# Optimization experiments

Measured on AMD Instinct MI355X. Metric: run time of the kernel, lower is better.

## Reference

```python
import jax, jax.numpy as jnp
import numpy as np
import math

HIDDEN = 1024
HEADS = 16
HEAD_DIM = HIDDEN // HEADS
B, S = 2, 2048


def setup_inputs() -> dict:
    key = jax.random.key(0)
    ks = jax.random.split(key, 10)
    std = 1.0 / math.sqrt(HIDDEN)
    mk = lambda k: (jax.random.normal(k, (HIDDEN, HIDDEN), jnp.float32) * std)
    return {
        "hidden_states": jax.random.normal(ks[0], (B, S, HIDDEN), jnp.float32),
        "attention_mask": jnp.zeros((B, 1, 1, S), jnp.float32),
        "wq": mk(ks[1]), "bq": jnp.zeros((HIDDEN,), jnp.float32),
        "wk": mk(ks[2]), "bk": jnp.zeros((HIDDEN,), jnp.float32),
        "wv": mk(ks[3]), "bv": jnp.zeros((HIDDEN,), jnp.float32),
        "wo": mk(ks[4]), "bo": jnp.zeros((HIDDEN,), jnp.float32),
    }


def reference(hidden_states, attention_mask, wq, bq, wk, bk, wv, bv, wo, bo):
    b, s, _ = hidden_states.shape
    scale = math.sqrt(HEAD_DIM)
    # projections (torch Linear: x @ W.T + b); weights stored as [out, in]
    q = hidden_states @ wq.T + bq
    k = hidden_states @ wk.T + bk
    v = hidden_states @ wv.T + bv
    # [B, H, S, D]
    q = q.reshape(b, s, HEADS, HEAD_DIM).transpose(0, 2, 1, 3)
    k = k.reshape(b, s, HEADS, HEAD_DIM).transpose(0, 2, 1, 3)
    v = v.reshape(b, s, HEADS, HEAD_DIM).transpose(0, 2, 1, 3)
    scores = jnp.einsum("bhqd,bhkd->bhqk", q, k) / scale
    scores = scores + attention_mask  # broadcast [B,1,1,S]
    weights = jax.nn.softmax(scores, axis=-1)  # dropout = identity (eval)
    out = jnp.einsum("bhqk,bhkd->bhqd", weights, v)
    out = out.transpose(0, 2, 1, 3).reshape(b, s, HIDDEN)
    out = out @ wo.T + bo
    return out
```

## Files before the change

kernel.cpp:

```cpp
#include <hip/hip_runtime.h>
#include <hip/hip_bf16.h>

typedef __bf16 bf16_t;
typedef __bf16 bf16x8 __attribute__((ext_vector_type(8)));
typedef _Float16 f16x4 __attribute__((ext_vector_type(4)));
typedef _Float16 f16x8 __attribute__((ext_vector_type(8)));
typedef float f32x4 __attribute__((ext_vector_type(4)));

#define SEQ    2048
#define NH     16
#define HD     64
#define HIDDEN 1024
#define LOG2E  1.44269504f
#define CSTR   41

__device__ __forceinline__ bf16_t to_bf16(float f) { return (bf16_t)f; }

__device__ __forceinline__ void async16(const void* g, void* l) {
    __builtin_amdgcn_global_load_lds((const __attribute__((address_space(1))) void*)g,
                                     (__attribute__((address_space(3))) void*)l, 16, 0, 0);
}

__global__ __launch_bounds__(256) void cvt_kernel(
    const float* __restrict__ s0, bf16_t* __restrict__ d0, int c0,
    const float* __restrict__ s1, bf16_t* __restrict__ d1, int c1,
    const float* __restrict__ s2, bf16_t* __restrict__ d2, int c2,
    const float* __restrict__ s3, bf16_t* __restrict__ d3, int c3,
    const float* __restrict__ s4, bf16_t* __restrict__ d4, int c4)
{
    int blk = blockIdx.x;
    const float* s; bf16_t* d;
    if (blk < c0)              { s = s0; d = d0; }
    else if ((blk -= c0) < c1) { s = s1; d = d1; }
    else if ((blk -= c1) < c2) { s = s2; d = d2; }
    else if ((blk -= c2) < c3) { s = s3; d = d3; }
    else                       { blk -= c3; s = s4; d = d4; }
    const size_t base = (size_t)blk * 2048 + threadIdx.x * 8;
    const float4 a = *(const float4*)&s[base];
    const float4 b = *(const float4*)&s[base + 4];
    bf16x8 o;
    o[0] = (bf16_t)a.x; o[1] = (bf16_t)a.y; o[2] = (bf16_t)a.z; o[3] = (bf16_t)a.w;
    o[4] = (bf16_t)b.x; o[5] = (bf16_t)b.y; o[6] = (bf16_t)b.z; o[7] = (bf16_t)b.w;
    *(bf16x8*)&d[base] = o;
}

__global__ __launch_bounds__(256, 3) void qkv_kernel(
    const bf16_t* __restrict__ X,
    const bf16_t* __restrict__ wq, const bf16_t* __restrict__ wk, const bf16_t* __restrict__ wv,
    const float* __restrict__ bq, const float* __restrict__ bk, const float* __restrict__ bv,
    bf16_t* __restrict__ qws, bf16_t* __restrict__ kws, _Float16* __restrict__ vws)
{
    __shared__ __align__(16) bf16_t Sh[16384];
    const int z = blockIdx.z;
    const bf16_t* Wsel = (z == 0) ? wq : (z == 1) ? wk : wv;
    const float*  bsel = (z == 0) ? bq : (z == 1) ? bk : bv;
    const int m0 = blockIdx.y * 128, n0 = blockIdx.x * 128;

    const int t = threadIdx.x, lane = t & 63, w = t >> 6;
    const int w0 = w & 1, w1 = w >> 1, l15 = lane & 15, q4 = lane >> 4;

    f32x4 acc[4][4];
#pragma unroll
    for (int i = 0; i < 4; i++)
#pragma unroll
        for (int j = 0; j < 4; j++) acc[i][j] = f32x4{0.f, 0.f, 0.f, 0.f};

    auto stage = [&](int kt, int buf) {
#pragma unroll
        for (int j = 0; j < 2; j++) {
            const int s = j * 256 + t;
            const int row = s >> 2, c = (s & 3) ^ (row & 3);
            const int lb = buf * 8192 + (j * 256 + w * 64) * 8;
            async16(&X[(size_t)(m0 + row) * HIDDEN + kt + c * 8], &Sh[lb]);
            async16(&Wsel[(size_t)(n0 + row) * HIDDEN + kt + c * 8], &Sh[lb + 4096]);
        }
    };
    stage(0, 0);

    for (int it = 0; it < 32; it++) {
        const int cur = it & 1;
        __syncthreads();
        if (it < 31) stage((it + 1) * 32, cur ^ 1);
        const bf16_t* As = &Sh[cur * 8192];
        const bf16_t* Bs = &Sh[cur * 8192 + 4096];
        bf16x8 af[4];
#pragma unroll
        for (int ti = 0; ti < 4; ti++) {
            const int ra = w0 * 64 + ti * 16 + l15;
            af[ti] = *(const bf16x8*)&As[ra * 32 + (q4 ^ (ra & 3)) * 8];
        }
#pragma unroll
        for (int tj = 0; tj < 4; tj++) {
            const int rb = w1 * 64 + tj * 16 + l15;
            const bf16x8 bfr = *(const bf16x8*)&Bs[rb * 32 + (q4 ^ (rb & 3)) * 8];
#pragma unroll
            for (int ti = 0; ti < 4; ti++)
                acc[ti][tj] = __builtin_amdgcn_mfma_f32_16x16x32_bf16(af[ti], bfr, acc[ti][tj], 0, 0, 0);
        }
    }
    __syncthreads();

    if (z < 2) {
#pragma unroll
        for (int tj = 0; tj < 4; tj++) {
            const int n = w1 * 64 + tj * 16 + l15;
            const float bb = bsel[n0 + n];
            const int ch = (n >> 3), sub = n & 7;
#pragma unroll
            for (int ti = 0; ti < 4; ti++)
#pragma unroll
                for (int r = 0; r < 4; r++) {
                    const int m = w0 * 64 + ti * 16 + q4 * 4 + r;
                    Sh[m * 128 + ((ch ^ (m & 15)) << 3) + sub] = to_bf16(acc[ti][tj][r] + bb);
                }
        }
        __syncthreads();
        bf16_t* dst = (z == 0) ? qws : kws;
#pragma unroll
        for (int i = 0; i < 8; i++) {
            const int g = i * 256 + t;
            const int row = g >> 4, c = g & 15;
            const bf16x8 vv = *(const bf16x8*)&Sh[row * 128 + ((c ^ (row & 15)) << 3)];
            *(bf16x8*)&dst[(size_t)(m0 + row) * HIDDEN + n0 + c * 8] = vv;
        }
    } else {
        _Float16* Vt = (_Float16*)Sh;
#pragma unroll
        for (int tj = 0; tj < 4; tj++) {
            const int n = w1 * 64 + tj * 16 + l15;
            const float bb = bsel[n0 + n];
#pragma unroll
            for (int ti = 0; ti < 4; ti++) {
                const int mb = w0 * 64 + ti * 16 + q4 * 4;
                f16x4 v;
#pragma unroll
                for (int r = 0; r < 4; r++) v[r] = (_Float16)(acc[ti][tj][r] + bb);
                *(f16x4*)&Vt[n * 128 + (((mb >> 3) ^ (n & 15)) << 3) + (mb & 7)] = v;
            }
        }
        __syncthreads();
        const int b = m0 >> 11, sbase = m0 & (SEQ - 1);
#pragma unroll
        for (int i = 0; i < 8; i++) {
            const int g = i * 256 + t;
            const int row = g >> 4, c = g & 15;
            const f16x8 vv = *(const f16x8*)&Vt[row * 128 + ((c ^ (row & 15)) << 3)];
            const int d = (n0 + row) & 63, hh = (n0 + row) >> 6;
            *(f16x8*)&vws[(((size_t)b * NH + hh) * HD + d) * SEQ + sbase + c * 8] = vv;
        }
    }
}

__global__ __launch_bounds__(256, 4) void attn_kernel(
    const bf16_t* __restrict__ Qw, const bf16_t* __restrict__ Kw,
    const _Float16* __restrict__ Vtw, const float* __restrict__ Mask,
    bf16_t* __restrict__ Ow)
{
    __shared__ __align__(16) bf16_t Tiles[2][2][64 * 64];

    const int t = threadIdx.x, lane = t & 63, w = t >> 6;
    const int l15 = lane & 15, q4 = lane >> 4;
    const int wq = w & 1, kh = w >> 1;
    const int lid = blockIdx.x;
    const int c8 = lid & 7, j = lid >> 3;
    const int bh = c8 * 4 + (j >> 5);
    const int q0 = (j & 31) * 64;
    const int b = bh >> 4, h = bh & 15;

    const bf16_t* Qh = Qw + (size_t)b * SEQ * HIDDEN + h * HD;
    const bf16_t* Kh = Kw + (size_t)b * SEQ * HIDDEN + h * HD;
    const _Float16* Vh = Vtw + (size_t)bh * HD * SEQ;
    const float* Mrow = Mask + (size_t)b * SEQ;

    bf16x8 qf[2][2];
#pragma unroll
    for (int nq = 0; nq < 2; nq++)
#pragma unroll
        for (int ks = 0; ks < 2; ks++)
            qf[nq][ks] = *(const bf16x8*)&Qh[(size_t)(q0 + wq * 32 + nq * 16 + l15) * HIDDEN + ks * 32 + q4 * 8];

    f32x4 oacc[2][4];
#pragma unroll
    for (int nq = 0; nq < 2; nq++)
#pragma unroll
        for (int nb = 0; nb < 4; nb++) oacc[nq][nb] = f32x4{0.f, 0.f, 0.f, 0.f};
    float psum[2] = {0.f, 0.f};

    bf16_t* Ksh = &Tiles[kh][0][0];
    _Float16* Vsh = (_Float16*)&Tiles[kh][1][0];
    const int kbase = kh * (SEQ / 2);
    const int s0_ = wq * 64 + lane;

    for (int it = 0; it < 16; it++) {
        const int kt = kbase + it * 64;
#pragma unroll
        for (int jj = 0; jj < 4; jj++) {
            const int s = jj * 128 + s0_;
            const int row = s >> 3, c = (s & 7) ^ (row & 7);
            const int lbase = (jj * 128 + wq * 64) * 8;
            async16(&Kh[(size_t)(kt + row) * HIDDEN + c * 8], &Ksh[lbase]);
            async16(&Vh[(size_t)row * SEQ + kt + c * 8], &Vsh[lbase]);
        }
        __syncthreads();

        f32x4 sa[2][4];
#pragma unroll
        for (int nq = 0; nq < 2; nq++)
#pragma unroll
            for (int cb = 0; cb < 4; cb++) sa[nq][cb] = f32x4{0.f, 0.f, 0.f, 0.f};
#pragma unroll
        for (int cb = 0; cb < 4; cb++)
#pragma unroll
            for (int ks = 0; ks < 2; ks++) {
                const int rk = cb * 16 + l15;
                const bf16x8 kf = *(const bf16x8*)&Ksh[rk * 64 + (((ks * 4 + q4) ^ (rk & 7))) * 8];
                sa[0][cb] = __builtin_amdgcn_mfma_f32_16x16x32_bf16(kf, qf[0][ks], sa[0][cb], 0, 0, 0);
                sa[1][cb] = __builtin_amdgcn_mfma_f32_16x16x32_bf16(kf, qf[1][ks], sa[1][cb], 0, 0, 0);
            }

        f16x4 ph[2][4];
#pragma unroll
        for (int cb = 0; cb < 4; cb++) {
            float4 mv = *(const float4*)&Mrow[kt + cb * 16 + q4 * 4];
            mv.x *= LOG2E; mv.y *= LOG2E; mv.z *= LOG2E; mv.w *= LOG2E;
            const float mk[4] = {mv.x, mv.y, mv.z, mv.w};
#pragma unroll
            for (int nq = 0; nq < 2; nq++) {
#pragma unroll
                for (int r = 0; r < 4; r++) {
                    const float p = exp2f(fmaf(sa[nq][cb][r], 0.125f * LOG2E, mk[r]));
                    psum[nq] += p;
                    ph[nq][cb][r] = (_Float16)p;
                }
            }
        }

#pragma unroll
        for (int cb = 0; cb < 4; cb++) {
#pragma unroll
            for (int nb = 0; nb < 4; nb++) {
                const int rv = nb * 16 + l15;
                const int cl = (cb * 2 + (q4 >> 1)) ^ (rv & 7);
                const f16x4 vf = *(const f16x4*)&Vsh[rv * 64 + cl * 8 + (q4 & 1) * 4];
                oacc[0][nb] = __builtin_amdgcn_mfma_f32_16x16x16f16(ph[0][cb], vf, oacc[0][nb], 0, 0, 0);
                oacc[1][nb] = __builtin_amdgcn_mfma_f32_16x16x16f16(ph[1][cb], vf, oacc[1][nb], 0, 0, 0);
            }
        }
        __syncthreads();
    }

#pragma unroll
    for (int nq = 0; nq < 2; nq++) {
        psum[nq] += __shfl_xor(psum[nq], 16);
        psum[nq] += __shfl_xor(psum[nq], 32);
    }

    float* Cb = (float*)&Tiles[0][0][0];
    const int crow = (wq * 64 + lane) * CSTR;
    if (kh == 1) {
#pragma unroll
        for (int nq = 0; nq < 2; nq++) {
#pragma unroll
            for (int nb = 0; nb < 4; nb++)
                *(f32x4*)&Cb[crow + (nq * 4 + nb) * 4] = oacc[nq][nb];
            Cb[crow + 32 + nq] = psum[nq];
        }
    }
    __syncthreads();
    if (kh == 0) {
#pragma unroll
        for (int nq = 0; nq < 2; nq++) {
#pragma unroll
            for (int nb = 0; nb < 4; nb++)
                oacc[nq][nb] += *(const f32x4*)&Cb[crow + (nq * 4 + nb) * 4];
            psum[nq] += Cb[crow + 32 + nq];
        }
#pragma unroll
        for (int nq = 0; nq < 2; nq++) {
            float inv[4];
#pragma unroll
            for (int r = 0; r < 4; r++) inv[r] = 1.f / __shfl(psum[nq], q4 * 4 + r);
#pragma unroll
            for (int r = 0; r < 4; r++) {
                const int s = q0 + wq * 32 + nq * 16 + q4 * 4 + r;
#pragma unroll
                for (int nb = 0; nb < 4; nb++)
                    Ow[((size_t)b * SEQ + s) * HIDDEN + h * HD + nb * 16 + l15] =
                        to_bf16(oacc[nq][nb][r] * inv[r]);
            }
        }
    }
}

__global__ __launch_bounds__(256, 2) void oproj_kernel(
    const bf16_t* __restrict__ A, const bf16_t* __restrict__ Wo,
    const float* __restrict__ bo, float* __restrict__ Out)
{
    __shared__ __align__(16) bf16_t Sh[12288];
    const int m0 = blockIdx.y * 64, n0 = blockIdx.x * 128;
    const int t = threadIdx.x, lane = t & 63, w = t >> 6;
    const int l15 = lane & 15, q4 = lane >> 4;

    f32x4 acc[4][2];
#pragma unroll
    for (int i = 0; i < 4; i++)
#pragma unroll
        for (int j = 0; j < 2; j++) acc[i][j] = f32x4{0.f, 0.f, 0.f, 0.f};

    auto stage = [&](int kt, int buf) {
        {
            const int row = t >> 2, c = (t & 3) ^ (row & 3);
            async16(&A[(size_t)(m0 + row) * HIDDEN + kt + c * 8], &Sh[buf * 6144 + w * 64 * 8]);
        }
#pragma unroll
        for (int j = 0; j < 2; j++) {
            const int s = j * 256 + t;
            const int row = s >> 2, c = (s & 3) ^ (row & 3);
            async16(&Wo[(size_t)(n0 + row) * HIDDEN + kt + c * 8],
                    &Sh[buf * 6144 + 2048 + (j * 256 + w * 64) * 8]);
        }
    };
    stage(0, 0);

    for (int it = 0; it < 32; it++) {
        const int cur = it & 1;
        __syncthreads();
        if (it < 31) stage((it + 1) * 32, cur ^ 1);
        const bf16_t* As = &Sh[cur * 6144];
        const bf16_t* Bs = &Sh[cur * 6144 + 2048];
        bf16x8 af[4];
#pragma unroll
        for (int ti = 0; ti < 4; ti++) {
            const int ra = ti * 16 + l15;
            af[ti] = *(const bf16x8*)&As[ra * 32 + (q4 ^ (ra & 3)) * 8];
        }
#pragma unroll
        for (int tj = 0; tj < 2; tj++) {
            const int rb = w * 32 + tj * 16 + l15;
            const bf16x8 bfr = *(const bf16x8*)&Bs[rb * 32 + (q4 ^ (rb & 3)) * 8];
#pragma unroll
            for (int ti = 0; ti < 4; ti++)
                acc[ti][tj] = __builtin_amdgcn_mfma_f32_16x16x32_bf16(bfr, af[ti], acc[ti][tj], 0, 0, 0);
        }
    }

#pragma unroll
    for (int tj = 0; tj < 2; tj++) {
        const int nb4 = n0 + w * 32 + tj * 16 + q4 * 4;
        const float4 bb = *(const float4*)&bo[nb4];
#pragma unroll
        for (int ti = 0; ti < 4; ti++) {
            const int m = m0 + ti * 16 + l15;
            float4 ov;
            ov.x = acc[ti][tj][0] + bb.x;
            ov.y = acc[ti][tj][1] + bb.y;
            ov.z = acc[ti][tj][2] + bb.z;
            ov.w = acc[ti][tj][3] + bb.w;
            *(float4*)&Out[(size_t)m * HIDDEN + nb4] = ov;
        }
    }
}

extern "C" void kernel_launch(void* const* d_in, const int* in_sizes, int n_in,
                              void* d_out, int out_size, void* d_ws, size_t ws_size,
                              hipStream_t stream) {
    const float* X   = (const float*)d_in[0];
    const float* msk = (const float*)d_in[1];
    const float* wq  = (const float*)d_in[2];
    const float* bq  = (const float*)d_in[3];
    const float* wk  = (const float*)d_in[4];
    const float* bk  = (const float*)d_in[5];
    const float* wv  = (const float*)d_in[6];
    const float* bv  = (const float*)d_in[7];
    const float* wo  = (const float*)d_in[8];
    const float* bo  = (const float*)d_in[9];
    float* out = (float*)d_out;

    const size_t NELT = (size_t)2 * SEQ * HIDDEN;
    const size_t WELT = (size_t)HIDDEN * HIDDEN;
    bf16_t*    xbf = (bf16_t*)d_ws;
    bf16_t*    qws = xbf + NELT;
    bf16_t*    kws = qws + NELT;
    _Float16*  vws = (_Float16*)(kws + NELT);
    bf16_t*    aws = xbf;
    bf16_t*    wqb = (bf16_t*)d_out;
    bf16_t*    wkb = wqb + WELT;
    bf16_t*    wvb = wkb + WELT;
    bf16_t*    wob = wvb + WELT;

    cvt_kernel<<<dim3(2048 + 4 * 512), dim3(256), 0, stream>>>(
        X, xbf, 2048, wq, wqb, 512, wk, wkb, 512, wv, wvb, 512, wo, wob, 512);
    qkv_kernel<<<dim3(8, 32, 3), dim3(256), 0, stream>>>(
        xbf, wqb, wkb, wvb, bq, bk, bv, qws, kws, vws);
    attn_kernel<<<dim3(1024), dim3(256), 0, stream>>>(qws, kws, vws, msk, aws);
    oproj_kernel<<<dim3(8, 64), dim3(256), 0, stream>>>(aws, wob, bo, out);
}
```

Baseline: 208.4 us.

## Fuse fp32 weight conversion into QKV and output-projection GEMM tile loads

```diff
diff --git a/kernel.cpp b/kernel.cpp
--- a/kernel.cpp
+++ b/kernel.cpp
@@ -21,39 +21,35 @@
                                      (__attribute__((address_space(3))) void*)l, 16, 0, 0);
 }
 
+__device__ __forceinline__ bf16x8 pack_bf16(const f32x4 a, const f32x4 b) {
+    bf16x8 o;
+    o[0] = (bf16_t)a[0]; o[1] = (bf16_t)a[1]; o[2] = (bf16_t)a[2]; o[3] = (bf16_t)a[3];
+    o[4] = (bf16_t)b[0]; o[5] = (bf16_t)b[1]; o[6] = (bf16_t)b[2]; o[7] = (bf16_t)b[3];
+    return o;
+}
+
 __global__ __launch_bounds__(256) void cvt_kernel(
-    const float* __restrict__ s0, bf16_t* __restrict__ d0, int c0,
-    const float* __restrict__ s1, bf16_t* __restrict__ d1, int c1,
-    const float* __restrict__ s2, bf16_t* __restrict__ d2, int c2,
-    const float* __restrict__ s3, bf16_t* __restrict__ d3, int c3,
-    const float* __restrict__ s4, bf16_t* __restrict__ d4, int c4)
+    const float* __restrict__ s0, bf16_t* __restrict__ d0)
 {
-    int blk = blockIdx.x;
-    const float* s; bf16_t* d;
-    if (blk < c0)              { s = s0; d = d0; }
-    else if ((blk -= c0) < c1) { s = s1; d = d1; }
-    else if ((blk -= c1) < c2) { s = s2; d = d2; }
-    else if ((blk -= c2) < c3) { s = s3; d = d3; }
-    else                       { blk -= c3; s = s4; d = d4; }
-    const size_t base = (size_t)blk * 2048 + threadIdx.x * 8;
-    const float4 a = *(const float4*)&s[base];
-    const float4 b = *(const float4*)&s[base + 4];
+    const size_t base = (size_t)blockIdx.x * 2048 + threadIdx.x * 8;
+    const float4 a = *(const float4*)&s0[base];
+    const float4 b = *(const float4*)&s0[base + 4];
     bf16x8 o;
     o[0] = (bf16_t)a.x; o[1] = (bf16_t)a.y; o[2] = (bf16_t)a.z; o[3] = (bf16_t)a.w;
     o[4] = (bf16_t)b.x; o[5] = (bf16_t)b.y; o[6] = (bf16_t)b.z; o[7] = (bf16_t)b.w;
-    *(bf16x8*)&d[base] = o;
+    *(bf16x8*)&d0[base] = o;
 }
 
 __global__ __launch_bounds__(256, 3) void qkv_kernel(
     const bf16_t* __restrict__ X,
-    const bf16_t* __restrict__ wq, const bf16_t* __restrict__ wk, const bf16_t* __restrict__ wv,
+    const float* __restrict__ wq, const float* __restrict__ wk, const float* __restrict__ wv,
     const float* __restrict__ bq, const float* __restrict__ bk, const float* __restrict__ bv,
     bf16_t* __restrict__ qws, bf16_t* __restrict__ kws, _Float16* __restrict__ vws)
 {
-    __shared__ __align__(16) bf16_t Sh[16384];
+    __shared__ __align__(16) bf16_t Sh[24576];
     const int z = blockIdx.z;
-    const bf16_t* Wsel = (z == 0) ? wq : (z == 1) ? wk : wv;
-    const float*  bsel = (z == 0) ? bq : (z == 1) ? bk : bv;
+    const float* Wsel = (z == 0) ? wq : (z == 1) ? wk : wv;
+    const float* bsel = (z == 0) ? bq : (z == 1) ? bk : bv;
     const int m0 = blockIdx.y * 128, n0 = blockIdx.x * 128;
 
     const int t = threadIdx.x, lane = t & 63, w = t >> 6;
@@ -69,10 +65,17 @@
 #pragma unroll
         for (int j = 0; j < 2; j++) {
             const int s = j * 256 + t;
-            const int row = s >> 2, c = (s & 3) ^ (row & 3);
-            const int lb = buf * 8192 + (j * 256 + w * 64) * 8;
-            async16(&X[(size_t)(m0 + row) * HIDDEN + kt + c * 8], &Sh[lb]);
-            async16(&Wsel[(size_t)(n0 + row) * HIDDEN + kt + c * 8], &Sh[lb + 4096]);
+            const int row = s >> 2, c = (s & 3) ^ ((row >> 1) & 3);
+            async16(&X[(size_t)(m0 + row) * HIDDEN + kt + c * 8],
+                    &Sh[buf * 12288 + (j * 256 + w * 64) * 8]);
+        }
+        float* Bf = (float*)&Sh[buf * 12288 + 4096];
+#pragma unroll
+        for (int j = 0; j < 4; j++) {
+            const int s = j * 256 + t;
+            const int row = s >> 3, c = (s & 7) ^ (row & 7);
+            async16(&Wsel[(size_t)(n0 + row) * HIDDEN + kt + c * 4],
+                    &Bf[(j * 256 + w * 64) * 4]);
         }
     };
     stage(0, 0);
@@ -81,18 +84,20 @@
         const int cur = it & 1;
         __syncthreads();
         if (it < 31) stage((it + 1) * 32, cur ^ 1);
-        const bf16_t* As = &Sh[cur * 8192];
-        const bf16_t* Bs = &Sh[cur * 8192 + 4096];
+        const bf16_t* As = &Sh[cur * 12288];
+        const float*  Bf = (const float*)&Sh[cur * 12288 + 4096];
         bf16x8 af[4];
 #pragma unroll
         for (int ti = 0; ti < 4; ti++) {
             const int ra = w0 * 64 + ti * 16 + l15;
-            af[ti] = *(const bf16x8*)&As[ra * 32 + (q4 ^ (ra & 3)) * 8];
+            af[ti] = *(const bf16x8*)&As[ra * 32 + (q4 ^ ((ra >> 1) & 3)) * 8];
         }
 #pragma unroll
         for (int tj = 0; tj < 4; tj++) {
             const int rb = w1 * 64 + tj * 16 + l15;
-            const bf16x8 bfr = *(const bf16x8*)&Bs[rb * 32 + (q4 ^ (rb & 3)) * 8];
+            const f32x4 b0 = *(const f32x4*)&Bf[rb * 32 + ((2 * q4)     ^ (rb & 7)) * 4];
+            const f32x4 b1 = *(const f32x4*)&Bf[rb * 32 + ((2 * q4 + 1) ^ (rb & 7)) * 4];
+            const bf16x8 bfr = pack_bf16(b0, b1);
 #pragma unroll
             for (int ti = 0; ti < 4; ti++)
                 acc[ti][tj] = __builtin_amdgcn_mfma_f32_16x16x32_bf16(af[ti], bfr, acc[ti][tj], 0, 0, 0);
@@ -292,32 +297,32 @@
     }
 }
 
-__global__ __launch_bounds__(256, 2) void oproj_kernel(
-    const bf16_t* __restrict__ A, const bf16_t* __restrict__ Wo,
+__global__ __launch_bounds__(256, 4) void oproj_kernel(
+    const bf16_t* __restrict__ A, const float* __restrict__ Wo,
     const float* __restrict__ bo, float* __restrict__ Out)
 {
     __shared__ __align__(16) bf16_t Sh[12288];
-    const int m0 = blockIdx.y * 64, n0 = blockIdx.x * 128;
+    const int m0 = blockIdx.y * 64, n0 = blockIdx.x * 64;
     const int t = threadIdx.x, lane = t & 63, w = t >> 6;
     const int l15 = lane & 15, q4 = lane >> 4;
 
-    f32x4 acc[4][2];
-#pragma unroll
-    for (int i = 0; i < 4; i++)
-#pragma unroll
-        for (int j = 0; j < 2; j++) acc[i][j] = f32x4{0.f, 0.f, 0.f, 0.f};
+    f32x4 acc[4];
+#pragma unroll
+    for (int i = 0; i < 4; i++) acc[i] = f32x4{0.f, 0.f, 0.f, 0.f};
 
     auto stage = [&](int kt, int buf) {
         {
-            const int row = t >> 2, c = (t & 3) ^ (row & 3);
-            async16(&A[(size_t)(m0 + row) * HIDDEN + kt + c * 8], &Sh[buf * 6144 + w * 64 * 8]);
-        }
+            const int row = t >> 2, c = (t & 3) ^ ((row >> 1) & 3);
+            async16(&A[(size_t)(m0 + row) * HIDDEN + kt + c * 8],
+                    &Sh[buf * 6144 + (w * 64) * 8]);
+        }
+        float* Bf = (float*)&Sh[buf * 6144 + 2048];
 #pragma unroll
         for (int j = 0; j < 2; j++) {
             const int s = j * 256 + t;
-            const int row = s >> 2, c = (s & 3) ^ (row & 3);
-            async16(&Wo[(size_t)(n0 + row) * HIDDEN + kt + c * 8],
-                    &Sh[buf * 6144 + 2048 + (j * 256 + w * 64) * 8]);
+            const int row = s >> 3, c = (s & 7) ^ (row & 7);
+            async16(&Wo[(size_t)(n0 + row) * HIDDEN + kt + c * 4],
+                    &Bf[(j * 256 + w * 64) * 4]);
         }
     };
     stage(0, 0);
@@ -327,37 +332,30 @@
         __syncthreads();
         if (it < 31) stage((it + 1) * 32, cur ^ 1);
         const bf16_t* As = &Sh[cur * 6144];
-        const bf16_t* Bs = &Sh[cur * 6144 + 2048];
-        bf16x8 af[4];
+        const float*  Bf = (const float*)&Sh[cur * 6144 + 2048];
+        const int rb = w * 16 + l15;
+        const f32x4 b0 = *(const f32x4*)&Bf[rb * 32 + ((2 * q4)     ^ (rb & 7)) * 4];
+        const f32x4 b1 = *(const f32x4*)&Bf[rb * 32 + ((2 * q4 + 1) ^ (rb & 7)) * 4];
+        const bf16x8 bfr = pack_bf16(b0, b1);
 #pragma unroll
         for (int ti = 0; ti < 4; ti++) {
             const int ra = ti * 16 + l15;
-            af[ti] = *(const bf16x8*)&As[ra * 32 + (q4 ^ (ra & 3)) * 8];
-        }
-#pragma unroll
-        for (int tj = 0; tj < 2; tj++) {
-            const int rb = w * 32 + tj * 16 + l15;
-            const bf16x8 bfr = *(const bf16x8*)&Bs[rb * 32 + (q4 ^ (rb & 3)) * 8];
-#pragma unroll
-            for (int ti = 0; ti < 4; ti++)
-                acc[ti][tj] = __builtin_amdgcn_mfma_f32_16x16x32_bf16(bfr, af[ti], acc[ti][tj], 0, 0, 0);
-        }
-    }
-
-#pragma unroll
-    for (int tj = 0; tj < 2; tj++) {
-        const int nb4 = n0 + w * 32 + tj * 16 + q4 * 4;
-        const float4 bb = *(const float4*)&bo[nb4];
-#pragma unroll
-        for (int ti = 0; ti < 4; ti++) {
-            const int m = m0 + ti * 16 + l15;
-            float4 ov;
-            ov.x = acc[ti][tj][0] + bb.x;
-            ov.y = acc[ti][tj][1] + bb.y;
-            ov.z = acc[ti][tj][2] + bb.z;
-            ov.w = acc[ti][tj][3] + bb.w;
-            *(float4*)&Out[(size_t)m * HIDDEN + nb4] = ov;
-        }
+            const bf16x8 af = *(const bf16x8*)&As[ra * 32 + (q4 ^ ((ra >> 1) & 3)) * 8];
+            acc[ti] = __builtin_amdgcn_mfma_f32_16x16x32_bf16(bfr, af, acc[ti], 0, 0, 0);
+        }
+    }
+
+    const int nb4 = n0 + w * 16 + q4 * 4;
+    const float4 bb = *(const float4*)&bo[nb4];
+#pragma unroll
+    for (int ti = 0; ti < 4; ti++) {
+        const int m = m0 + ti * 16 + l15;
+        float4 ov;
+        ov.x = acc[ti][0] + bb.x;
+        ov.y = acc[ti][1] + bb.y;
+        ov.z = acc[ti][2] + bb.z;
+        ov.w = acc[ti][3] + bb.w;
+        *(float4*)&Out[(size_t)m * HIDDEN + nb4] = ov;
     }
 }
 
@@ -377,21 +375,15 @@
     float* out = (float*)d_out;
 
     const size_t NELT = (size_t)2 * SEQ * HIDDEN;
-    const size_t WELT = (size_t)HIDDEN * HIDDEN;
     bf16_t*    xbf = (bf16_t*)d_ws;
     bf16_t*    qws = xbf + NELT;
     bf16_t*    kws = qws + NELT;
     _Float16*  vws = (_Float16*)(kws + NELT);
     bf16_t*    aws = xbf;
-    bf16_t*    wqb = (bf16_t*)d_out;
-    bf16_t*    wkb = wqb + WELT;
-    bf16_t*    wvb = wkb + WELT;
-    bf16_t*    wob = wvb + WELT;
-
-    cvt_kernel<<<dim3(2048 + 4 * 512), dim3(256), 0, stream>>>(
-        X, xbf, 2048, wq, wqb, 512, wk, wkb, 512, wv, wvb, 512, wo, wob, 512);
+
+    cvt_kernel<<<dim3(2048), dim3(256), 0, stream>>>(X, xbf);
     qkv_kernel<<<dim3(8, 32, 3), dim3(256), 0, stream>>>(
-        xbf, wqb, wkb, wvb, bq, bk, bv, qws, kws, vws);
+        xbf, wq, wk, wv, bq, bk, bv, qws, kws, vws);
     attn_kernel<<<dim3(1024), dim3(256), 0, stream>>>(qws, kws, vws, msk, aws);
-    oproj_kernel<<<dim3(8, 64), dim3(256), 0, stream>>>(aws, wob, bo, out);
-}
+    oproj_kernel<<<dim3(16, 64), dim3(256), 0, stream>>>(aws, wo, bo, out);
+}
```

Result: slower. 220.6 us (+5.9%).
